# Kernel tuning notes

Hardware: AMD Instinct MI355X
Metric: run time of the kernel (lower is better)

## Reference

```python
import jax, jax.numpy as jnp
import numpy as np
import math

WINDOW = 257
W = (WINDOW - 1) // 2      # 128
Q_CH = WINDOW + 1          # 258 (query chunk size / stride)
K_CH = WINDOW * 2          # 514 (key window size)


def compl_mod(m, n):
    return int(n * math.ceil(m / n) - m)


def setup_inputs() -> dict:
    key = jax.random.key(0)
    k1, k2, k3 = jax.random.split(key, 3)
    b, s, nh, h = 2, 4096, 16, 64
    q = jax.random.normal(k1, (b, s, nh, h), jnp.float32)
    k = jax.random.normal(k2, (b, s, nh, h), jnp.float32)
    v = jax.random.normal(k3, (b, s, nh, h), jnp.float32)
    return {"q": q, "k": k, "v": v}


def reference(q, k, v):
    b, s, nh, h = q.shape
    q = q * h ** (-0.5)
    q_pad = compl_mod(s, Q_CH)
    k_pad = compl_mod(s + 2 * W - K_CH, Q_CH)
    c = (s + q_pad) // Q_CH  # number of chunks

    # pad along sequence dim (q right-padded; k/v haloed by w on both sides)
    qp = jnp.pad(q, ((0, 0), (0, q_pad), (0, 0), (0, 0)))
    kp = jnp.pad(k, ((0, 0), (W, W + k_pad), (0, 0), (0, 0)))
    vp = jnp.pad(v, ((0, 0), (W, W + k_pad), (0, 0), (0, 0)))

    # unfold: q non-overlapping chunks, k/v overlapping windows (size K_CH, stride Q_CH)
    qw = qp.reshape(b, c, Q_CH, nh, h)                              # [b,c,q,nh,h]
    idx = (jnp.arange(c) * Q_CH)[:, None] + jnp.arange(K_CH)[None]  # [c,K_CH]
    kw = kp[:, idx]                                                 # [b,c,k,nh,h]
    vw = vp[:, idx]

    A = jnp.einsum('bcqnh,bcknh->bncqk', qw, kw)  # [b,nh,c,Q_CH,K_CH]

    # banded mask: valid iff i <= j <= i + 2w (True = masked)
    i = jnp.arange(Q_CH)[:, None]
    j = jnp.arange(K_CH)[None, :]
    base = ~((j >= i) & (j <= i + 2 * W))
    mask_left = base.at[:, :W].set(True)                    # first chunk: no left halo
    mask_right = base.at[:, K_CH - (W + k_pad):].set(True)  # last chunk: no right halo/pad
    if c > 1:
        mask = jnp.concatenate(
            [mask_left[None], jnp.broadcast_to(base, (c - 2, Q_CH, K_CH)), mask_right[None]], axis=0)
    else:
        mask = (mask_left | mask_right)[None]

    mask_value = -jnp.finfo(A.dtype).max
    A = jnp.where(mask[None, None], mask_value, A)
    A = jax.nn.softmax(A, axis=-1)  # dropout omitted (eval mode)

    z = jnp.einsum('bncqk,bcknh->bncqh', A, vw)       # [b,nh,c,Q_CH,h]
    z = z.reshape(b, nh, c * Q_CH, h)[:, :, :s]       # trim q padding
    return jnp.transpose(z, (0, 2, 1, 3))             # [b,s,nh,h]
```

## Files before the change

### kernel.cpp

```cpp
#include <hip/hip_runtime.h>

typedef _Float16 h16;
typedef __attribute__((ext_vector_type(2))) _Float16 f16x2;
typedef __attribute__((ext_vector_type(4))) _Float16 f16x4;
typedef __attribute__((ext_vector_type(2))) __fp16   fp16x2n;
typedef __attribute__((ext_vector_type(8))) _Float16 f16x8;
typedef __attribute__((ext_vector_type(4))) float f32x4;
typedef __attribute__((ext_vector_type(4))) int   i32x4;

#define S_LEN 4096
#define NHEAD 16
#define HDIM  64
#define WIN   128
#define TQ    128
#define NQT   (S_LEN / TQ)
#define NCHT  12
#define KSTR  72
#define VSTR2 40
#define QSCALE 0.18033688011112042f

static __device__ __forceinline__ f16x2 pk(float a, float b) {
    fp16x2n r = __builtin_amdgcn_cvt_pkrtz(a, b);
    return __builtin_bit_cast(f16x2, r);
}

static __device__ __forceinline__ f16x8 cvt8(float4 a, float4 b) {
    f16x2 p0 = pk(a.x, a.y), p1 = pk(a.z, a.w);
    f16x2 p2 = pk(b.x, b.y), p3 = pk(b.z, b.w);
    f16x8 r;
    r[0]=p0[0]; r[1]=p0[1]; r[2]=p1[0]; r[3]=p1[1];
    r[4]=p2[0]; r[5]=p2[1]; r[6]=p3[0]; r[7]=p3[1];
    return r;
}

__global__ __launch_bounds__(512, 4)
void wattn(const float* __restrict__ Qg, const float* __restrict__ Kg,
           const float* __restrict__ Vg, float* __restrict__ Og)
{
    __shared__ h16 Kbuf[3][32 * KSTR];
    __shared__ h16 Vbuf[3][64 * VSTR2];

    const int tid  = threadIdx.x;
    const int wid  = tid >> 6;
    const int lane = tid & 63;
    const int l15  = lane & 15;
    const int quad = lane >> 4;

    int lin = blockIdx.x + NQT * (blockIdx.y + NHEAD * blockIdx.z);
    int nwg = NQT * NHEAD * gridDim.z;
    int swz = ((nwg & 7) == 0) ? ((lin & 7) * (nwg >> 3) + (lin >> 3)) : lin;
    const int bx   = swz & (NQT - 1);
    const int head = (swz / NQT) & (NHEAD - 1);
    const int b    = swz / (NQT * NHEAD);

    const int q0    = bx * TQ;
    const int kbase = q0 - WIN;
    const int rowstride = NHEAD * HDIM;

    const float* KB = Kg + ((long)b * S_LEN * NHEAD + head) * HDIM;
    const float* VB = Vg + ((long)b * S_LEN * NHEAD + head) * HDIM;

    const int srow = tid >> 4;
    const int ish  = tid & 15;
    const int sh0  = ish * 4;
    const int vkey = ((srow + (((ish >> 2) & 3) << 3)) & 31) ^ ((ish & 3) << 3);

    float4 kreg, vreg;
    #define SLOAD(i) do {                                                    \
        int kg_ = kbase + (i)*32 + srow;                                     \
        kg_ = kg_ < 0 ? 0 : (kg_ > S_LEN-1 ? S_LEN-1 : kg_);                 \
        const float* kp_ = KB + (long)kg_ * rowstride + sh0;                 \
        const float* vp_ = VB + (long)kg_ * rowstride + sh0;                 \
        kreg = *(const float4*)kp_;                                          \
        vreg = *(const float4*)vp_;                                          \
    } while (0)
    #define SWRITE(i) do {                                                   \
        int bi_ = (i) % 3;                                                   \
        f16x2 ka_ = pk(kreg.x, kreg.y), kb_ = pk(kreg.z, kreg.w);            \
        f16x4 kv_; kv_[0]=ka_[0]; kv_[1]=ka_[1]; kv_[2]=kb_[0]; kv_[3]=kb_[1];\
        *(f16x4*)&Kbuf[bi_][srow * KSTR + sh0] = kv_;                        \
        Vbuf[bi_][(sh0+0) * VSTR2 + vkey] = (h16)vreg.x;                     \
        Vbuf[bi_][(sh0+1) * VSTR2 + vkey] = (h16)vreg.y;                     \
        Vbuf[bi_][(sh0+2) * VSTR2 + vkey] = (h16)vreg.z;                     \
        Vbuf[bi_][(sh0+3) * VSTR2 + vkey] = (h16)vreg.w;                     \
    } while (0)

    SLOAD(0);

    f16x8 aQ0, aQ1;
    {
        const int qrow = q0 + wid * 16 + l15;
        const float* qp = Qg + ((long)(b * S_LEN + qrow) * NHEAD + head) * HDIM;
        float4 x0 = *(const float4*)(qp + quad*8);
        float4 x1 = *(const float4*)(qp + quad*8 + 4);
        float4 x2 = *(const float4*)(qp + 32 + quad*8);
        float4 x3 = *(const float4*)(qp + 32 + quad*8 + 4);
        x0.x*=QSCALE; x0.y*=QSCALE; x0.z*=QSCALE; x0.w*=QSCALE;
        x1.x*=QSCALE; x1.y*=QSCALE; x1.z*=QSCALE; x1.w*=QSCALE;
        x2.x*=QSCALE; x2.y*=QSCALE; x2.z*=QSCALE; x2.w*=QSCALE;
        x3.x*=QSCALE; x3.y*=QSCALE; x3.z*=QSCALE; x3.w*=QSCALE;
        aQ0 = cvt8(x0, x1);
        aQ1 = cvt8(x2, x3);
    }

    SWRITE(0);
    SLOAD(1);
    __syncthreads();

    const int qg = q0 + wid*16 + l15;
    const int lo = (qg - WIN < 0) ? 0 : qg - WIN;
    const int hi = (qg + WIN > S_LEN-1) ? S_LEN-1 : qg + WIN;
    const unsigned span = (unsigned)(hi - lo);

    float l_lane = 0.f;
    f32x4 Oacc[4];
    #pragma unroll
    for (int t = 0; t < 4; ++t) Oacc[t] = (f32x4){0.f,0.f,0.f,0.f};

    const int c0 = wid >> 1;
    const int pxr = (l15 & 12) << 1;
    const int xl = (quad == 1 || quad == 2) ? (lane ^ 48) : lane;

    for (int i = 0; i < NCHT; ++i) {
        if (i + 1 < NCHT) SWRITE(i + 1);
        if (i + 2 < NCHT) SLOAD(i + 2);

        if ((unsigned)(i - c0) < 9u) {
            const h16* Kb = Kbuf[i % 3];
            const h16* Vb = Vbuf[i % 3];

            f16x8 bK00 = *(const f16x8*)&Kb[ l15      * KSTR + quad*8];
            f16x8 bK01 = *(const f16x8*)&Kb[ l15      * KSTR + 32 + quad*8];
            f16x8 bK10 = *(const f16x8*)&Kb[(16+l15)  * KSTR + quad*8];
            f16x8 bK11 = *(const f16x8*)&Kb[(16+l15)  * KSTR + 32 + quad*8];

            f32x4 s0 = (f32x4){0.f,0.f,0.f,0.f};
            s0 = __builtin_amdgcn_mfma_f32_16x16x32_f16(bK00, aQ0, s0, 0, 0, 0);
            s0 = __builtin_amdgcn_mfma_f32_16x16x32_f16(bK01, aQ1, s0, 0, 0, 0);
            f32x4 s1 = (f32x4){0.f,0.f,0.f,0.f};
            s1 = __builtin_amdgcn_mfma_f32_16x16x32_f16(bK10, aQ0, s1, 0, 0, 0);
            s1 = __builtin_amdgcn_mfma_f32_16x16x32_f16(bK11, aQ1, s1, 0, 0, 0);

            const int colb = kbase + i*32 + quad*4;
            float pl[4], ph[4];
            #pragma unroll
            for (int r = 0; r < 4; ++r) {
                int c_ = colb + r;
                float v0 = ((unsigned)(c_      - lo) <= span) ? s0[r] : -1e30f;
                float v1 = ((unsigned)(c_ + 16 - lo) <= span) ? s1[r] : -1e30f;
                pl[r] = exp2f(v0);
                ph[r] = exp2f(v1);
            }
            l_lane += ((pl[0]+pl[1]) + (pl[2]+pl[3]))
                    + ((ph[0]+ph[1]) + (ph[2]+ph[3]));

            int u0 = __builtin_bit_cast(int, pk(pl[0], pl[1]));
            int u1 = __builtin_bit_cast(int, pk(pl[2], pl[3]));
            int u2 = __builtin_bit_cast(int, pk(ph[0], ph[1]));
            int u3 = __builtin_bit_cast(int, pk(ph[2], ph[3]));
            {
                const bool q0b = (quad & 1);
                int s0w = q0b ? u0 : u2;
                int s1w = q0b ? u1 : u3;
                int r0 = __builtin_amdgcn_ds_swizzle(s0w, 0x401F);
                int r1 = __builtin_amdgcn_ds_swizzle(s1w, 0x401F);
                if (q0b) { u0 = r0; u1 = r1; } else { u2 = r0; u3 = r1; }
            }
            u0 = __shfl(u0, xl);  u1 = __shfl(u1, xl);
            u2 = __shfl(u2, xl);  u3 = __shfl(u3, xl);
            i32x4 uu; uu[0]=u0; uu[1]=u1; uu[2]=u2; uu[3]=u3;
            f16x8 aP = __builtin_bit_cast(f16x8, uu);

            #pragma unroll
            for (int t = 0; t < 4; ++t) {
                f16x8 bV = *(const f16x8*)&Vb[(t*16 + l15) * VSTR2 +
                                              (((quad*8 + (t << 3)) & 31) ^ pxr)];
                Oacc[t] = __builtin_amdgcn_mfma_f32_16x16x32_f16(aP, bV, Oacc[t], 0, 0, 0);
            }
        }

        __syncthreads();
    }
    #undef SLOAD
    #undef SWRITE

    float l = l_lane;
    l += __shfl_xor(l, 16);
    l += __shfl_xor(l, 32);
    const float inv = 1.0f / l;

    float* op = Og + ((long)(b * S_LEN + q0 + wid*16) * NHEAD + head) * HDIM;
    #pragma unroll
    for (int r = 0; r < 4; ++r) {
        float invr = __shfl(inv, quad*4 + r);
        #pragma unroll
        for (int t = 0; t < 4; ++t) {
            op[(quad*4 + r) * rowstride + t*16 + l15] = Oacc[t][r] * invr;
        }
    }
}

extern "C" void kernel_launch(void* const* d_in, const int* in_sizes, int n_in,
                              void* d_out, int out_size, void* d_ws, size_t ws_size,
                              hipStream_t stream) {
    const float* q = (const float*)d_in[0];
    const float* k = (const float*)d_in[1];
    const float* v = (const float*)d_in[2];
    float* out = (float*)d_out;
    const int batch = in_sizes[0] / (S_LEN * NHEAD * HDIM);
    dim3 grid(NQT, NHEAD, batch);
    wattn<<<grid, 512, 0, stream>>>(q, k, v, out);
}
```

Baseline: 148.3 us.

## Double query tile per workgroup so each warp reuses K/V fragments for two row-tiles

Each block now covers 256 queries instead of 128, and each warp handles two 16-row query tiles. The K and V fragments read from shared memory are reused across both tiles' MFMAs. This cuts redundant global K/V halo loads, since 16 chunks serve 256 queries instead of 12 chunks serving 128, and it halves shared-memory reads per MFMA. The cost is more registers per thread, half as many workgroups, and a longer serial chunk loop per block, which may reduce occupancy and parallelism.

```diff
diff --git a/kernel.cpp b/kernel.cpp
--- a/kernel.cpp
+++ b/kernel.cpp
@@ -12,9 +12,9 @@
 #define NHEAD 16
 #define HDIM  64
 #define WIN   128
-#define TQ    128
+#define TQ    256
 #define NQT   (S_LEN / TQ)
-#define NCHT  12
+#define NCH   16
 #define KSTR  72
 #define VSTR2 40
 #define QSCALE 0.18033688011112042f
@@ -87,9 +87,10 @@
 
     SLOAD(0);
 
-    f16x8 aQ0, aQ1;
-    {
-        const int qrow = q0 + wid * 16 + l15;
+    f16x8 aQ[2][2];
+    #pragma unroll
+    for (int t2 = 0; t2 < 2; ++t2) {
+        const int qrow = q0 + wid*32 + t2*16 + l15;
         const float* qp = Qg + ((long)(b * S_LEN + qrow) * NHEAD + head) * HDIM;
         float4 x0 = *(const float4*)(qp + quad*8);
         float4 x1 = *(const float4*)(qp + quad*8 + 4);
@@ -99,83 +100,103 @@
         x1.x*=QSCALE; x1.y*=QSCALE; x1.z*=QSCALE; x1.w*=QSCALE;
         x2.x*=QSCALE; x2.y*=QSCALE; x2.z*=QSCALE; x2.w*=QSCALE;
         x3.x*=QSCALE; x3.y*=QSCALE; x3.z*=QSCALE; x3.w*=QSCALE;
-        aQ0 = cvt8(x0, x1);
-        aQ1 = cvt8(x2, x3);
+        aQ[t2][0] = cvt8(x0, x1);
+        aQ[t2][1] = cvt8(x2, x3);
     }
 
     SWRITE(0);
     SLOAD(1);
     __syncthreads();
 
-    const int qg = q0 + wid*16 + l15;
-    const int lo = (qg - WIN < 0) ? 0 : qg - WIN;
-    const int hi = (qg + WIN > S_LEN-1) ? S_LEN-1 : qg + WIN;
-    const unsigned span = (unsigned)(hi - lo);
-
-    float l_lane = 0.f;
-    f32x4 Oacc[4];
-    #pragma unroll
-    for (int t = 0; t < 4; ++t) Oacc[t] = (f32x4){0.f,0.f,0.f,0.f};
-
-    const int c0 = wid >> 1;
+    int lo[2]; unsigned span[2];
+    #pragma unroll
+    for (int t2 = 0; t2 < 2; ++t2) {
+        const int qg = q0 + wid*32 + t2*16 + l15;
+        lo[t2] = (qg - WIN < 0) ? 0 : qg - WIN;
+        const int hi = (qg + WIN > S_LEN-1) ? S_LEN-1 : qg + WIN;
+        span[t2] = (unsigned)(hi - lo[t2]);
+    }
+
+    float l_lane[2] = {0.f, 0.f};
+    f32x4 Oacc[2][4];
+    #pragma unroll
+    for (int t2 = 0; t2 < 2; ++t2)
+        #pragma unroll
+        for (int t = 0; t < 4; ++t) Oacc[t2][t] = (f32x4){0.f,0.f,0.f,0.f};
+
     const int pxr = (l15 & 12) << 1;
     const int xl = (quad == 1 || quad == 2) ? (lane ^ 48) : lane;
 
-    for (int i = 0; i < NCHT; ++i) {
-        if (i + 1 < NCHT) SWRITE(i + 1);
-        if (i + 2 < NCHT) SLOAD(i + 2);
-
-        if ((unsigned)(i - c0) < 9u) {
+    for (int i = 0; i < NCH; ++i) {
+        if (i + 1 < NCH) SWRITE(i + 1);
+        if (i + 2 < NCH) SLOAD(i + 2);
+
+        if ((unsigned)(i - wid) < 9u) {
             const h16* Kb = Kbuf[i % 3];
             const h16* Vb = Vbuf[i % 3];
 
-            f16x8 bK00 = *(const f16x8*)&Kb[ l15      * KSTR + quad*8];
-            f16x8 bK01 = *(const f16x8*)&Kb[ l15      * KSTR + 32 + quad*8];
-            f16x8 bK10 = *(const f16x8*)&Kb[(16+l15)  * KSTR + quad*8];
-            f16x8 bK11 = *(const f16x8*)&Kb[(16+l15)  * KSTR + 32 + quad*8];
-
-            f32x4 s0 = (f32x4){0.f,0.f,0.f,0.f};
-            s0 = __builtin_amdgcn_mfma_f32_16x16x32_f16(bK00, aQ0, s0, 0, 0, 0);
-            s0 = __builtin_amdgcn_mfma_f32_16x16x32_f16(bK01, aQ1, s0, 0, 0, 0);
-            f32x4 s1 = (f32x4){0.f,0.f,0.f,0.f};
-            s1 = __builtin_amdgcn_mfma_f32_16x16x32_f16(bK10, aQ0, s1, 0, 0, 0);
-            s1 = __builtin_amdgcn_mfma_f32_16x16x32_f16(bK11, aQ1, s1, 0, 0, 0);
-
+            f32x4 s0[2], s1[2];
+            {
+                f16x8 bK00 = *(const f16x8*)&Kb[ l15      * KSTR + quad*8];
+                f16x8 bK01 = *(const f16x8*)&Kb[ l15      * KSTR + 32 + quad*8];
+                #pragma unroll
+                for (int t2 = 0; t2 < 2; ++t2) {
+                    f32x4 z = (f32x4){0.f,0.f,0.f,0.f};
+                    z = __builtin_amdgcn_mfma_f32_16x16x32_f16(bK00, aQ[t2][0], z, 0, 0, 0);
+                    z = __builtin_amdgcn_mfma_f32_16x16x32_f16(bK01, aQ[t2][1], z, 0, 0, 0);
+                    s0[t2] = z;
+                }
+                f16x8 bK10 = *(const f16x8*)&Kb[(16+l15)  * KSTR + quad*8];
+                f16x8 bK11 = *(const f16x8*)&Kb[(16+l15)  * KSTR + 32 + quad*8];
+                #pragma unroll
+                for (int t2 = 0; t2 < 2; ++t2) {
+                    f32x4 z = (f32x4){0.f,0.f,0.f,0.f};
+                    z = __builtin_amdgcn_mfma_f32_16x16x32_f16(bK10, aQ[t2][0], z, 0, 0, 0);
+                    z = __builtin_amdgcn_mfma_f32_16x16x32_f16(bK11, aQ[t2][1], z, 0, 0, 0);
+                    s1[t2] = z;
+                }
+            }
+
+            f16x8 aP[2];
             const int colb = kbase + i*32 + quad*4;
-            float pl[4], ph[4];
             #pragma unroll
-            for (int r = 0; r < 4; ++r) {
-                int c_ = colb + r;
-                float v0 = ((unsigned)(c_      - lo) <= span) ? s0[r] : -1e30f;
-                float v1 = ((unsigned)(c_ + 16 - lo) <= span) ? s1[r] : -1e30f;
-                pl[r] = exp2f(v0);
-                ph[r] = exp2f(v1);
-            }
-            l_lane += ((pl[0]+pl[1]) + (pl[2]+pl[3]))
-                    + ((ph[0]+ph[1]) + (ph[2]+ph[3]));
-
-            int u0 = __builtin_bit_cast(int, pk(pl[0], pl[1]));
-            int u1 = __builtin_bit_cast(int, pk(pl[2], pl[3]));
-            int u2 = __builtin_bit_cast(int, pk(ph[0], ph[1]));
-            int u3 = __builtin_bit_cast(int, pk(ph[2], ph[3]));
-            {
-                const bool q0b = (quad & 1);
-                int s0w = q0b ? u0 : u2;
-                int s1w = q0b ? u1 : u3;
-                int r0 = __builtin_amdgcn_ds_swizzle(s0w, 0x401F);
-                int r1 = __builtin_amdgcn_ds_swizzle(s1w, 0x401F);
-                if (q0b) { u0 = r0; u1 = r1; } else { u2 = r0; u3 = r1; }
-            }
-            u0 = __shfl(u0, xl);  u1 = __shfl(u1, xl);
-            u2 = __shfl(u2, xl);  u3 = __shfl(u3, xl);
-            i32x4 uu; uu[0]=u0; uu[1]=u1; uu[2]=u2; uu[3]=u3;
-            f16x8 aP = __builtin_bit_cast(f16x8, uu);
+            for (int t2 = 0; t2 < 2; ++t2) {
+                float pl[4], ph[4];
+                #pragma unroll
+                for (int r = 0; r < 4; ++r) {
+                    int c_ = colb + r;
+                    float v0 = ((unsigned)(c_      - lo[t2]) <= span[t2]) ? s0[t2][r] : -1e30f;
+                    float v1 = ((unsigned)(c_ + 16 - lo[t2]) <= span[t2]) ? s1[t2][r] : -1e30f;
+                    pl[r] = exp2f(v0);
+                    ph[r] = exp2f(v1);
+                }
+                l_lane[t2] += ((pl[0]+pl[1]) + (pl[2]+pl[3]))
+                            + ((ph[0]+ph[1]) + (ph[2]+ph[3]));
+
+                int u0 = __builtin_bit_cast(int, pk(pl[0], pl[1]));
+                int u1 = __builtin_bit_cast(int, pk(pl[2], pl[3]));
+                int u2 = __builtin_bit_cast(int, pk(ph[0], ph[1]));
+                int u3 = __builtin_bit_cast(int, pk(ph[2], ph[3]));
+                {
+                    const bool q0b = (quad & 1);
+                    int s0w = q0b ? u0 : u2;
+                    int s1w = q0b ? u1 : u3;
+                    int r0 = __builtin_amdgcn_ds_swizzle(s0w, 0x401F);
+                    int r1 = __builtin_amdgcn_ds_swizzle(s1w, 0x401F);
+                    if (q0b) { u0 = r0; u1 = r1; } else { u2 = r0; u3 = r1; }
+                }
+                u0 = __shfl(u0, xl);  u1 = __shfl(u1, xl);
+                u2 = __shfl(u2, xl);  u3 = __shfl(u3, xl);
+                i32x4 uu; uu[0]=u0; uu[1]=u1; uu[2]=u2; uu[3]=u3;
+                aP[t2] = __builtin_bit_cast(f16x8, uu);
+            }
 
             #pragma unroll
             for (int t = 0; t < 4; ++t) {
                 f16x8 bV = *(const f16x8*)&Vb[(t*16 + l15) * VSTR2 +
                                               (((quad*8 + (t << 3)) & 31) ^ pxr)];
-                Oacc[t] = __builtin_amdgcn_mfma_f32_16x16x32_f16(aP, bV, Oacc[t], 0, 0, 0);
+                Oacc[0][t] = __builtin_amdgcn_mfma_f32_16x16x32_f16(aP[0], bV, Oacc[0][t], 0, 0, 0);
+                Oacc[1][t] = __builtin_amdgcn_mfma_f32_16x16x32_f16(aP[1], bV, Oacc[1][t], 0, 0, 0);
             }
         }
 
@@ -184,18 +205,21 @@
     #undef SLOAD
     #undef SWRITE
 
-    float l = l_lane;
-    l += __shfl_xor(l, 16);
-    l += __shfl_xor(l, 32);
-    const float inv = 1.0f / l;
-
-    float* op = Og + ((long)(b * S_LEN + q0 + wid*16) * NHEAD + head) * HDIM;
-    #pragma unroll
-    for (int r = 0; r < 4; ++r) {
-        float invr = __shfl(inv, quad*4 + r);
+    #pragma unroll
+    for (int t2 = 0; t2 < 2; ++t2) {
+        float l = l_lane[t2];
+        l += __shfl_xor(l, 16);
+        l += __shfl_xor(l, 32);
+        const float inv = 1.0f / l;
+
+        float* op = Og + ((long)(b * S_LEN + q0 + wid*32 + t2*16) * NHEAD + head) * HDIM;
         #pragma unroll
-        for (int t = 0; t < 4; ++t) {
-            op[(quad*4 + r) * rowstride + t*16 + l15] = Oacc[t][r] * invr;
+        for (int r = 0; r < 4; ++r) {
+            float invr = __shfl(inv, quad*4 + r);
+            #pragma unroll
+            for (int t = 0; t < 4; ++t) {
+                op[(quad*4 + r) * rowstride + t*16 + l15] = Oacc[t2][t][r] * invr;
+            }
         }
     }
 }
```

New measurement: 148.7 us. No clear change (+0.3%).
